# Kernel optimization log

Measured on AMD Instinct MI355X. Metric: run time of the kernel, lower is better.

Reference implementation:

```python
import jax, jax.numpy as jnp
import numpy as np

S = 2048      # total packed tokens
E = 1152      # hidden_size (SigLIP)
H = 16        # num_attention_heads
D = E // H    # head_dim = 72
NSEG = 4      # number of packed image segments


def rotate_half(x):
    half = x.shape[-1] // 2
    return jnp.concatenate([-x[..., half:], x[..., :half]], axis=-1)


def setup_inputs() -> dict:
    key = jax.random.key(0)
    ks = jax.random.split(key, 10)
    init = lambda k, sh: jax.random.normal(k, sh, dtype=jnp.float32) * 0.02
    hidden_states = jax.random.normal(ks[0], (S, E), dtype=jnp.float32)
    q_w, k_w, v_w, o_w = (init(ks[i], (E, E)) for i in range(1, 5))
    q_b, k_b, v_b, o_b = (init(ks[i], (E,)) for i in range(5, 9))
    # rotary position embeddings over head_dim
    pos = jnp.arange(S, dtype=jnp.float32)
    inv_freq = 1.0 / (10000.0 ** (jnp.arange(0, D, 2, dtype=jnp.float32) / D))
    freqs = pos[:, None] * inv_freq[None, :]             # [S, D/2]
    emb = jnp.concatenate([freqs, freqs], axis=-1)       # [S, D]
    cos, sin = jnp.cos(emb), jnp.sin(emb)
    cu_seqlens = (jnp.arange(NSEG + 1) * (S // NSEG)).astype(jnp.int32)
    return dict(hidden_states=hidden_states, q_w=q_w, q_b=q_b, k_w=k_w, k_b=k_b,
                v_w=v_w, v_b=v_b, o_w=o_w, o_b=o_b, cos=cos, sin=sin,
                cu_seqlens=cu_seqlens)


def reference(hidden_states, q_w, q_b, k_w, k_b, v_w, v_b, o_w, o_b, cos, sin, cu_seqlens):
    seq_len, embed_dim = hidden_states.shape
    scaling = D ** -0.5
    q = (hidden_states @ q_w.T + q_b).reshape(seq_len, H, D)
    k = (hidden_states @ k_w.T + k_b).reshape(seq_len, H, D)
    v = (hidden_states @ v_w.T + v_b).reshape(seq_len, H, D)
    # RoPE in float32 (matches apply_rotary_pos_emb_vision); cos/sin broadcast over heads
    cos_e = cos.astype(jnp.float32)[:, None, :]  # [S, 1, D]
    sin_e = sin.astype(jnp.float32)[:, None, :]
    qf, kf = q.astype(jnp.float32), k.astype(jnp.float32)
    q = (qf * cos_e + rotate_half(qf) * sin_e).astype(q.dtype)
    k = (kf * cos_e + rotate_half(kf) * sin_e).astype(k.dtype)
    # block-diagonal (varlen) attention: token i attends only within its segment
    seg = jnp.searchsorted(cu_seqlens, jnp.arange(seq_len), side='right')  # [S]
    mask = seg[:, None] == seg[None, :]                                    # [S, S]
    scores = jnp.einsum('qhd,khd->hqk', q, k) * scaling                    # [H, S, S]
    scores = jnp.where(mask[None, :, :], scores, jnp.finfo(jnp.float32).min)
    weights = jax.nn.softmax(scores.astype(jnp.float32), axis=-1).astype(q.dtype)
    attn = jnp.einsum('hqk,khd->qhd', weights, v).reshape(seq_len, embed_dim)
    return attn @ o_w.T + o_b
```

## Files before the change

kernel.cpp:

```cpp
#include <hip/hip_runtime.h>

#define S 2048
#define E 1152
#define H 16
#define NSEG 4

typedef unsigned short u16;
typedef short bf16x8 __attribute__((ext_vector_type(8)));
typedef float f32x4 __attribute__((ext_vector_type(4)));

#define MFMA __builtin_amdgcn_mfma_f32_16x16x32_bf16

__device__ __forceinline__ u16 f2bf(float x) {
    unsigned u = __float_as_uint(x);
    u += 0x7fffu + ((u >> 16) & 1u);
    return (u16)(u >> 16);
}
__device__ __forceinline__ float bf2f(u16 h) {
    return __uint_as_float(((unsigned)h) << 16);
}
__device__ __forceinline__ bf16x8 ldb8(const u16* p) {
    return *(const bf16x8*)p;
}
__device__ __forceinline__ void gll16(const void* g, void* s) {
    __builtin_amdgcn_global_load_lds(
        (const __attribute__((address_space(1))) void*)g,
        (__attribute__((address_space(3))) void*)s,
        16, 0, 0);
}

__global__ __launch_bounds__(256)
void convert_inputs(const float* __restrict__ hs, const float* __restrict__ wq,
                    const float* __restrict__ wk, const float* __restrict__ wv,
                    const float* __restrict__ wo,
                    u16* __restrict__ hs_h, u16* __restrict__ wq_h,
                    u16* __restrict__ wk_h, u16* __restrict__ wv_h,
                    u16* __restrict__ wo_h)
{
    const size_t NH = (size_t)S * E, NW = (size_t)E * E;
    size_t i = ((size_t)blockIdx.x * 256 + threadIdx.x) * 4;
    const float* src; u16* dst; size_t off;
    if      (i < NH)          { src = hs; dst = hs_h; off = i; }
    else if (i < NH + NW)     { src = wq; dst = wq_h; off = i - NH; }
    else if (i < NH + 2*NW)   { src = wk; dst = wk_h; off = i - NH - NW; }
    else if (i < NH + 3*NW)   { src = wv; dst = wv_h; off = i - NH - 2*NW; }
    else if (i < NH + 4*NW)   { src = wo; dst = wo_h; off = i - NH - 3*NW; }
    else return;
    float4 v = *(const float4*)(src + off);
    ushort4 hv;
    hv.x = f2bf(v.x); hv.y = f2bf(v.y); hv.z = f2bf(v.z); hv.w = f2bf(v.w);
    *(ushort4*)(dst + off) = hv;
}

__global__ __launch_bounds__(256)
void gemm_qkv_f(const u16* __restrict__ hsb, const u16* __restrict__ wcat,
                const float* __restrict__ qb, const float* __restrict__ kb,
                const float* __restrict__ vb,
                u16* __restrict__ qbf, u16* __restrict__ kbf, u16* __restrict__ vt)
{
    __shared__ u16 As[2][128 * 64] __attribute__((aligned(16)));
    __shared__ u16 Bs[2][128 * 64] __attribute__((aligned(16)));
    const int tid = threadIdx.x;
    const int l = tid & 63, w = tid >> 6;
    const int wr = w >> 1, wc = w & 1;
    const int m0 = blockIdx.y * 128;
    const int n0 = blockIdx.x * 128;
    const int lr = l & 15, lk = (l >> 4) * 8;
    const int swz = (lr & 7) << 3;

    const int srow = tid >> 3;
    const int scol = ((tid & 7) ^ ((tid >> 3) & 7)) * 8;
    const u16* ga = hsb  + (size_t)(m0 + srow) * E + scol;
    const u16* gb = wcat + (size_t)(n0 + srow) * E + scol;
    const int ldst = w * 512;

    f32x4 acc[4][4] = {};

#define QKV_STAGE(buf, kt)                                              \
    {                                                                   \
        const u16* _a = ga + (kt) * 64;                                 \
        const u16* _b = gb + (kt) * 64;                                 \
        _Pragma("unroll")                                               \
        for (int r = 0; r < 4; ++r) {                                   \
            gll16(_a + (size_t)r * 32 * E, &As[buf][ldst + r * 2048]);  \
            gll16(_b + (size_t)r * 32 * E, &Bs[buf][ldst + r * 2048]);  \
        }                                                               \
    }

    QKV_STAGE(0, 0);
    __syncthreads();
    int cur = 0;
    for (int kt = 0; kt < 18; ++kt) {
        if (kt + 1 < 18) QKV_STAGE(cur ^ 1, kt + 1);
        const u16* Ab = As[cur];
        const u16* Bb = Bs[cur];
#pragma unroll
        for (int kk = 0; kk < 2; ++kk) {
            const int csw = (kk * 32 + lk) ^ swz;
            bf16x8 af[4], bfr[4];
#pragma unroll
            for (int i = 0; i < 4; ++i) {
                af[i]  = ldb8(Ab + (wr * 64 + i * 16 + lr) * 64 + csw);
                bfr[i] = ldb8(Bb + (wc * 64 + i * 16 + lr) * 64 + csw);
            }
#pragma unroll
            for (int i = 0; i < 4; ++i)
#pragma unroll
                for (int j = 0; j < 4; ++j)
                    acc[i][j] = MFMA(af[i], bfr[j], acc[i][j], 0, 0, 0);
        }
        __syncthreads();
        cur ^= 1;
    }

    const int zb = n0 / E;
    const int ncol = n0 - zb * E;
    const float* bias = (zb == 0) ? qb : (zb == 1) ? kb : vb;
    u16* qk = (zb == 0) ? qbf : kbf;
#pragma unroll
    for (int i = 0; i < 4; ++i) {
        int rbase = m0 + wr * 64 + i * 16 + (l >> 4) * 4;
#pragma unroll
        for (int j = 0; j < 4; ++j) {
            int cc = ncol + wc * 64 + j * 16 + lr;
            int hh = cc / 72, d = cc - hh * 72;
#pragma unroll
            for (int r = 0; r < 4; ++r) {
                float val = acc[i][j][r] + bias[cc];
                if (zb < 2) {
                    qk[((size_t)hh * S + rbase + r) * 96 + d] = f2bf(val);
                } else {
                    vt[((size_t)hh * 80 + d) * S + rbase + r] = f2bf(val);
                }
            }
        }
    }
}

__global__ __launch_bounds__(256)
void rope_convert(u16* __restrict__ qbf, u16* __restrict__ kbf,
                  const float* __restrict__ cosp, const float* __restrict__ sinp,
                  u16* __restrict__ vt)
{
    int idx = blockIdx.x * 256 + threadIdx.x;
    if (idx >= S * H * 36) return;
    int d = idx % 36;
    int h = (idx / 36) % H;
    int s = idx / (36 * H);
    float c = cosp[s * 72 + d], sn = sinp[s * 72 + d];
    size_t base = ((size_t)h * S + s) * 96;
    float q0 = bf2f(qbf[base + d]), q1 = bf2f(qbf[base + d + 36]);
    float k0 = bf2f(kbf[base + d]), k1 = bf2f(kbf[base + d + 36]);
    const float qs = 0.17002330685923512f;
    qbf[base + d]      = f2bf((q0 * c - q1 * sn) * qs);
    qbf[base + d + 36] = f2bf((q1 * c + q0 * sn) * qs);
    kbf[base + d]      = f2bf(k0 * c - k1 * sn);
    kbf[base + d + 36] = f2bf(k1 * c + k0 * sn);
    if (d < 24) { qbf[base + 72 + d] = 0; kbf[base + 72 + d] = 0; }
    if (d < 8)  { vt[((size_t)h * 80 + 72 + d) * S + s] = 0; }
}

__device__ __forceinline__ void loadK(bf16x8 (&kf)[12], const u16* kp) {
#pragma unroll
    for (int nt = 0; nt < 4; ++nt)
#pragma unroll
        for (int ks = 0; ks < 3; ++ks)
            kf[nt * 3 + ks] = ldb8(kp + nt * 16 * 96 + ks * 32);
}
__device__ __forceinline__ void loadV(bf16x8 (&vf)[10], const u16* vp) {
#pragma unroll
    for (int nt = 0; nt < 5; ++nt)
#pragma unroll
        for (int ks = 0; ks < 2; ++ks)
            vf[nt * 2 + ks] = ldb8(vp + (size_t)nt * 16 * S + ks * 32);
}
__device__ __forceinline__ void qkStep(f32x4 (&sc)[4], const bf16x8 (&qfr)[3],
                                       const bf16x8 (&kf)[12]) {
#pragma unroll
    for (int nt = 0; nt < 4; ++nt) {
        sc[nt] = f32x4{0.f, 0.f, 0.f, 0.f};
#pragma unroll
        for (int ks = 0; ks < 3; ++ks)
            sc[nt] = MFMA(qfr[ks], kf[nt * 3 + ks], sc[nt], 0, 0, 0);
    }
}
__device__ __forceinline__ void pvBody(const f32x4 (&sc)[4], float (&lsum)[4],
                                       const bf16x8 (&vf)[10], f32x4 (&oacc)[5],
                                       u16 (*pl)[72], int l) {
    const int lr = l & 15, g = l >> 4;
#pragma unroll
    for (int nt = 0; nt < 4; ++nt)
#pragma unroll
        for (int r = 0; r < 4; ++r) {
            float p = __builtin_amdgcn_exp2f(sc[nt][r]);
            unsigned pu = __float_as_uint(p) & 0xffff0000u;
            lsum[r] += __uint_as_float(pu);
            pl[g * 4 + r][lr + nt * 16] = (u16)(pu >> 16);
        }
    const int koff = g * 8;
#pragma unroll
    for (int ks = 0; ks < 2; ++ks) {
        bf16x8 pf = ldb8(&pl[lr][ks * 32 + koff]);
#pragma unroll
        for (int nt = 0; nt < 5; ++nt)
            oacc[nt] = MFMA(pf, vf[nt * 2 + ks], oacc[nt], 0, 0, 0);
    }
}

__global__ __launch_bounds__(256, 2)
void attn_mfma(const u16* __restrict__ qbf, const u16* __restrict__ kbf,
               const u16* __restrict__ vt, u16* __restrict__ ao,
               const int* __restrict__ cu)
{
    __shared__ u16 p_lds[4][16][72] __attribute__((aligned(16)));
    const int b = blockIdx.x;
    const int sid = (b & 7) * 64 + (b >> 3);
    const int h = sid >> 5;
    const int q0 = (sid & 31) * 64;
    const int l = threadIdx.x & 63, w = threadIdx.x >> 6;

    int kstart = 0, kend = S;
#pragma unroll
    for (int i = 0; i < NSEG; ++i) {
        int a = cu[i], b2 = cu[i + 1];
        if (q0 >= a && q0 < b2) { kstart = a; kend = b2; }
    }

    const int lr = l & 15;
    const int koff = (l >> 4) * 8;
    const u16* kbase = kbf + ((size_t)h * S + lr) * 96 + koff;
    const u16* vbase = vt + ((size_t)h * 80 + lr) * S + koff;

    bf16x8 qfr[3];
#pragma unroll
    for (int ks = 0; ks < 3; ++ks)
        qfr[ks] = ldb8(qbf + ((size_t)h * S + q0 + w * 16 + lr) * 96 + ks * 32 + koff);

    f32x4 oacc[5] = {};
    float lsum[4] = {0.f, 0.f, 0.f, 0.f};

    bf16x8 kfA[12], kfB[12], vfA[10], vfB[10];
    loadK(kfA, kbase + (size_t)kstart * 96);
    loadV(vfA, vbase + kstart);

    const int nch = (kend - kstart) >> 6;
    for (int c = 0; c < nch; c += 2) {
        const int kv0 = kstart + c * 64;
        f32x4 sc[4];
        qkStep(sc, qfr, kfA);
        if (c + 1 < nch) {
            loadK(kfB, kbase + (size_t)(kv0 + 64) * 96);
            loadV(vfB, vbase + kv0 + 64);
        }
        pvBody(sc, lsum, vfA, oacc, p_lds[w], l);
        if (c + 1 < nch) {
            qkStep(sc, qfr, kfB);
            if (c + 2 < nch) {
                loadK(kfA, kbase + (size_t)(kv0 + 128) * 96);
                loadV(vfA, vbase + kv0 + 128);
            }
            pvBody(sc, lsum, vfB, oacc, p_lds[w], l);
        }
    }

#pragma unroll
    for (int r = 0; r < 4; ++r) {
        float t = lsum[r];
        t += __shfl_xor(t, 1);
        t += __shfl_xor(t, 2);
        t += __shfl_xor(t, 4);
        t += __shfl_xor(t, 8);
        float inv = 1.0f / t;
        int srow = q0 + w * 16 + (l >> 4) * 4 + r;
#pragma unroll
        for (int nt = 0; nt < 5; ++nt) {
            int d = nt * 16 + lr;
            if (d < 72)
                ao[(size_t)srow * E + h * 72 + d] = f2bf(oacc[nt][r] * inv);
        }
    }
}

__global__ __launch_bounds__(256)
void gemm_o(const u16* __restrict__ ao, const u16* __restrict__ wo,
            const float* __restrict__ bias, float* __restrict__ out)
{
    __shared__ u16 As[2][64 * 64]  __attribute__((aligned(16)));
    __shared__ u16 Bs[2][128 * 64] __attribute__((aligned(16)));
    const int tid = threadIdx.x;
    const int l = tid & 63, w = tid >> 6;
    const int wr = w >> 1, wc = w & 1;
    const int bid = blockIdx.x;
    const int sid = (bid & 7) * 36 + (bid >> 3);
    const int m0 = (sid / 9) * 64;
    const int n0 = (sid % 9) * 128;
    const int lr = l & 15, lk = (l >> 4) * 8;
    const int swz = (lr & 7) << 3;

    const int srow = tid >> 3;
    const int scol = ((tid & 7) ^ ((tid >> 3) & 7)) * 8;
    const u16* ga = ao + (size_t)(m0 + srow) * E + scol;
    const u16* gb = wo + (size_t)(n0 + srow) * E + scol;
    const int ldst = w * 512;

    f32x4 acc[2][4] = {};

#define O_STAGE(buf, kt)                                                \
    {                                                                   \
        const u16* _a = ga + (kt) * 64;                                 \
        const u16* _b = gb + (kt) * 64;                                 \
        _Pragma("unroll")                                               \
        for (int r = 0; r < 2; ++r)                                     \
            gll16(_a + (size_t)r * 32 * E, &As[buf][ldst + r * 2048]);  \
        _Pragma("unroll")                                               \
        for (int r = 0; r < 4; ++r)                                     \
            gll16(_b + (size_t)r * 32 * E, &Bs[buf][ldst + r * 2048]);  \
    }

    O_STAGE(0, 0);
    __syncthreads();
    int cur = 0;
    for (int kt = 0; kt < 18; ++kt) {
        if (kt + 1 < 18) O_STAGE(cur ^ 1, kt + 1);
        const u16* Ab = As[cur];
        const u16* Bb = Bs[cur];
#pragma unroll
        for (int kk = 0; kk < 2; ++kk) {
            const int csw = (kk * 32 + lk) ^ swz;
            bf16x8 fa[2], fb[4];
#pragma unroll
            for (int i = 0; i < 2; ++i)
                fa[i] = ldb8(Ab + (wr * 32 + i * 16 + lr) * 64 + csw);
#pragma unroll
            for (int j = 0; j < 4; ++j)
                fb[j] = ldb8(Bb + (wc * 64 + j * 16 + lr) * 64 + csw);
#pragma unroll
            for (int i = 0; i < 2; ++i)
#pragma unroll
                for (int j = 0; j < 4; ++j)
                    acc[i][j] = MFMA(fa[i], fb[j], acc[i][j], 0, 0, 0);
        }
        __syncthreads();
        cur ^= 1;
    }
#pragma unroll
    for (int i = 0; i < 2; ++i) {
        int rbase = m0 + wr * 32 + i * 16 + (l >> 4) * 4;
#pragma unroll
        for (int j = 0; j < 4; ++j) {
            int cc = n0 + wc * 64 + j * 16 + lr;
#pragma unroll
            for (int r = 0; r < 4; ++r)
                out[(size_t)(rbase + r) * E + cc] = acc[i][j][r] + bias[cc];
        }
    }
}

extern "C" void kernel_launch(void* const* d_in, const int* in_sizes, int n_in,
                              void* d_out, int out_size, void* d_ws, size_t ws_size,
                              hipStream_t stream)
{
    const float* hs   = (const float*)d_in[0];
    const float* q_w  = (const float*)d_in[1];
    const float* q_b  = (const float*)d_in[2];
    const float* k_w  = (const float*)d_in[3];
    const float* k_b  = (const float*)d_in[4];
    const float* v_w  = (const float*)d_in[5];
    const float* v_b  = (const float*)d_in[6];
    const float* o_w  = (const float*)d_in[7];
    const float* o_b  = (const float*)d_in[8];
    const float* cosp = (const float*)d_in[9];
    const float* sinp = (const float*)d_in[10];
    const int*   cu   = (const int*)d_in[11];
    float* out = (float*)d_out;

    char* p = (char*)d_ws;
    u16* hs_h = (u16*)p; p += (size_t)S * E * 2;
    u16* wq_h = (u16*)p; p += (size_t)E * E * 2;
    u16* wk_h = (u16*)p; p += (size_t)E * E * 2;
    u16* wv_h = (u16*)p; p += (size_t)E * E * 2;
    u16* wo_h = (u16*)p; p += (size_t)E * E * 2;
    u16* qbf = (u16*)p; p += (size_t)H * S * 96 * 2;
    u16* kbf = (u16*)p; p += (size_t)H * S * 96 * 2;
    u16* vt  = (u16*)p; p += (size_t)H * 80 * S * 2;
    u16* ao  = (u16*)p; p += (size_t)S * E * 2;

    convert_inputs<<<7488, 256, 0, stream>>>(hs, q_w, k_w, v_w, o_w,
                                             hs_h, wq_h, wk_h, wv_h, wo_h);
    dim3 gq(27, 16);
    gemm_qkv_f<<<gq, 256, 0, stream>>>(hs_h, wq_h, q_b, k_b, v_b, qbf, kbf, vt);
    rope_convert<<<(S * H * 36) / 256, 256, 0, stream>>>(qbf, kbf, cosp, sinp, vt);
    attn_mfma<<<512, 256, 0, stream>>>(qbf, kbf, vt, ao, cu);
    gemm_o<<<288, 256, 0, stream>>>(ao, wo_h, o_b, out);
}
```

Before: 111.7 us.

## Stage K/V tiles through swizzled LDS with async global-to-LDS double buffering

The attention kernel no longer has every wave load its own K and V fragments from global memory into registers. The block now cooperatively copies each 64-key K/V chunk into double-buffered, XOR-swizzled shared memory using direct global-to-LDS loads, and the waves read their MFMA operands from there. This removes the four-fold redundant global loads and frees a large set of registers. In exchange it adds a block-wide barrier per chunk and about 45KB of LDS, and the launch bound no longer requests two blocks per CU, which may lower occupancy.

```diff
diff --git a/kernel.cpp b/kernel.cpp
--- a/kernel.cpp
+++ b/kernel.cpp
@@ -160,64 +160,22 @@
     if (d < 8)  { vt[((size_t)h * 80 + 72 + d) * S + s] = 0; }
 }
 
-__device__ __forceinline__ void loadK(bf16x8 (&kf)[12], const u16* kp) {
-#pragma unroll
-    for (int nt = 0; nt < 4; ++nt)
-#pragma unroll
-        for (int ks = 0; ks < 3; ++ks)
-            kf[nt * 3 + ks] = ldb8(kp + nt * 16 * 96 + ks * 32);
-}
-__device__ __forceinline__ void loadV(bf16x8 (&vf)[10], const u16* vp) {
-#pragma unroll
-    for (int nt = 0; nt < 5; ++nt)
-#pragma unroll
-        for (int ks = 0; ks < 2; ++ks)
-            vf[nt * 2 + ks] = ldb8(vp + (size_t)nt * 16 * S + ks * 32);
-}
-__device__ __forceinline__ void qkStep(f32x4 (&sc)[4], const bf16x8 (&qfr)[3],
-                                       const bf16x8 (&kf)[12]) {
-#pragma unroll
-    for (int nt = 0; nt < 4; ++nt) {
-        sc[nt] = f32x4{0.f, 0.f, 0.f, 0.f};
-#pragma unroll
-        for (int ks = 0; ks < 3; ++ks)
-            sc[nt] = MFMA(qfr[ks], kf[nt * 3 + ks], sc[nt], 0, 0, 0);
-    }
-}
-__device__ __forceinline__ void pvBody(const f32x4 (&sc)[4], float (&lsum)[4],
-                                       const bf16x8 (&vf)[10], f32x4 (&oacc)[5],
-                                       u16 (*pl)[72], int l) {
-    const int lr = l & 15, g = l >> 4;
-#pragma unroll
-    for (int nt = 0; nt < 4; ++nt)
-#pragma unroll
-        for (int r = 0; r < 4; ++r) {
-            float p = __builtin_amdgcn_exp2f(sc[nt][r]);
-            unsigned pu = __float_as_uint(p) & 0xffff0000u;
-            lsum[r] += __uint_as_float(pu);
-            pl[g * 4 + r][lr + nt * 16] = (u16)(pu >> 16);
-        }
-    const int koff = g * 8;
-#pragma unroll
-    for (int ks = 0; ks < 2; ++ks) {
-        bf16x8 pf = ldb8(&pl[lr][ks * 32 + koff]);
-#pragma unroll
-        for (int nt = 0; nt < 5; ++nt)
-            oacc[nt] = MFMA(pf, vf[nt * 2 + ks], oacc[nt], 0, 0, 0);
-    }
-}
-
-__global__ __launch_bounds__(256, 2)
+__global__ __launch_bounds__(256)
 void attn_mfma(const u16* __restrict__ qbf, const u16* __restrict__ kbf,
                const u16* __restrict__ vt, u16* __restrict__ ao,
                const int* __restrict__ cu)
 {
+    __shared__ u16 Kl[2][64 * 96] __attribute__((aligned(16)));
+    __shared__ u16 Vl[2][80 * 64] __attribute__((aligned(16)));
     __shared__ u16 p_lds[4][16][72] __attribute__((aligned(16)));
+
     const int b = blockIdx.x;
     const int sid = (b & 7) * 64 + (b >> 3);
     const int h = sid >> 5;
     const int q0 = (sid & 31) * 64;
     const int l = threadIdx.x & 63, w = threadIdx.x >> 6;
+    const int lr = l & 15, g = l >> 4;
+    const int koff = g * 8;
 
     int kstart = 0, kend = S;
 #pragma unroll
@@ -226,11 +184,6 @@
         if (q0 >= a && q0 < b2) { kstart = a; kend = b2; }
     }
 
-    const int lr = l & 15;
-    const int koff = (l >> 4) * 8;
-    const u16* kbase = kbf + ((size_t)h * S + lr) * 96 + koff;
-    const u16* vbase = vt + ((size_t)h * 80 + lr) * S + koff;
-
     bf16x8 qfr[3];
 #pragma unroll
     for (int ks = 0; ks < 3; ++ks)
@@ -239,28 +192,80 @@
     f32x4 oacc[5] = {};
     float lsum[4] = {0.f, 0.f, 0.f, 0.f};
 
-    bf16x8 kfA[12], kfB[12], vfA[10], vfB[10];
-    loadK(kfA, kbase + (size_t)kstart * 96);
-    loadV(vfA, vbase + kstart);
+#define ATTN_STAGE(buf, kv0_)                                                \
+    {                                                                        \
+        _Pragma("unroll")                                                    \
+        for (int uu = 0; uu < 6; ++uu) {                                     \
+            const int u = w + uu * 4;                                        \
+            if (u < 22) {                                                    \
+                const int f = u << 10;                                       \
+                if (u < 12) {                                                \
+                    int fb = f + l * 16;                                     \
+                    int row = fb / 192;                                      \
+                    int slot = (fb % 192) >> 4;                              \
+                    int gs = slot < 8 ? (slot ^ (row & 7))                   \
+                                      : (8 + ((slot & 3) ^ (row & 3)));      \
+                    gll16(kbf + ((size_t)h * S + (kv0_) + row) * 96 + gs * 8,\
+                          (char*)&Kl[buf][0] + f);                           \
+                } else {                                                     \
+                    int fb = (f - 12288) + l * 16;                           \
+                    int d = fb >> 7;                                         \
+                    int slot = (fb & 127) >> 4;                              \
+                    int gs = slot ^ (d & 7);                                 \
+                    gll16(vt + ((size_t)h * 80 + d) * S + (kv0_) + gs * 8,   \
+                          (char*)&Vl[buf][0] + (f - 12288));                 \
+                }                                                            \
+            }                                                                \
+        }                                                                    \
+    }
+
+#define ATTN_COMP(buf)                                                       \
+    {                                                                        \
+        f32x4 sc[4];                                                         \
+        _Pragma("unroll")                                                    \
+        for (int nt = 0; nt < 4; ++nt) {                                     \
+            sc[nt] = f32x4{0.f, 0.f, 0.f, 0.f};                              \
+            const int row = nt * 16 + lr;                                    \
+            _Pragma("unroll")                                                \
+            for (int ks = 0; ks < 3; ++ks) {                                 \
+                const int G = ks * 4 + g;                                    \
+                const int gsw = G < 8 ? (G ^ (lr & 7))                       \
+                                      : (8 + ((G & 3) ^ (lr & 3)));          \
+                bf16x8 kfr = ldb8(&Kl[buf][row * 96 + gsw * 8]);             \
+                sc[nt] = MFMA(qfr[ks], kfr, sc[nt], 0, 0, 0);                \
+            }                                                                \
+        }                                                                    \
+        _Pragma("unroll")                                                    \
+        for (int nt = 0; nt < 4; ++nt)                                       \
+            _Pragma("unroll")                                                \
+            for (int r = 0; r < 4; ++r) {                                    \
+                float pv = __builtin_amdgcn_exp2f(sc[nt][r]);                \
+                unsigned pu = __float_as_uint(pv) & 0xffff0000u;             \
+                lsum[r] += __uint_as_float(pu);                              \
+                p_lds[w][g * 4 + r][lr + nt * 16] = (u16)(pu >> 16);         \
+            }                                                                \
+        _Pragma("unroll")                                                    \
+        for (int ks = 0; ks < 2; ++ks) {                                     \
+            bf16x8 pf = ldb8(&p_lds[w][lr][ks * 32 + koff]);                 \
+            _Pragma("unroll")                                                \
+            for (int nt = 0; nt < 5; ++nt) {                                 \
+                const int vrow = nt * 16 + lr;                               \
+                const int vsl = (ks * 4 + g) ^ (lr & 7);                     \
+                bf16x8 vf = ldb8(&Vl[buf][vrow * 64 + vsl * 8]);             \
+                oacc[nt] = MFMA(pf, vf, oacc[nt], 0, 0, 0);                  \
+            }                                                                \
+        }                                                                    \
+    }
 
     const int nch = (kend - kstart) >> 6;
-    for (int c = 0; c < nch; c += 2) {
-        const int kv0 = kstart + c * 64;
-        f32x4 sc[4];
-        qkStep(sc, qfr, kfA);
-        if (c + 1 < nch) {
-            loadK(kfB, kbase + (size_t)(kv0 + 64) * 96);
-            loadV(vfB, vbase + kv0 + 64);
-        }
-        pvBody(sc, lsum, vfA, oacc, p_lds[w], l);
-        if (c + 1 < nch) {
-            qkStep(sc, qfr, kfB);
-            if (c + 2 < nch) {
-                loadK(kfA, kbase + (size_t)(kv0 + 128) * 96);
-                loadV(vfA, vbase + kv0 + 128);
-            }
-            pvBody(sc, lsum, vfB, oacc, p_lds[w], l);
-        }
+    ATTN_STAGE(0, kstart);
+    __syncthreads();
+    int cur = 0;
+    for (int c = 0; c < nch; ++c) {
+        if (c + 1 < nch) ATTN_STAGE(cur ^ 1, kstart + (c + 1) * 64);
+        ATTN_COMP(cur);
+        __syncthreads();
+        cur ^= 1;
     }
 
 #pragma unroll
@@ -271,7 +276,7 @@
         t += __shfl_xor(t, 4);
         t += __shfl_xor(t, 8);
         float inv = 1.0f / t;
-        int srow = q0 + w * 16 + (l >> 4) * 4 + r;
+        int srow = q0 + w * 16 + g * 4 + r;
 #pragma unroll
         for (int nt = 0; nt < 5; ++nt) {
             int d = nt * 16 + lr;
```

After: 94.90 us. 1.18x faster.
